# Performance work log

Measured on AMD Instinct MI355X. Metric: run time of the kernel, lower is better.

## Reference

```python
import jax, jax.numpy as jnp
import numpy as np

K = 3          # kernel_size (local window)
PAD = 1        # padding = (K-1)//2 -> 'same' output size
GROUPS = 8
C_OUT = 64


def _unfold3d(x, k):
    """x: [B,C,Dp,Hp,Wp] -> [B,C,D,H,W,kd,kh,kw] sliding windows (stride 1)."""
    B, C, Dp, Hp, Wp = x.shape
    D, H, W = Dp - k + 1, Hp - k + 1, Wp - k + 1
    idx_d = jnp.arange(D)[:, None] + jnp.arange(k)[None, :]
    idx_h = jnp.arange(H)[:, None] + jnp.arange(k)[None, :]
    idx_w = jnp.arange(W)[:, None] + jnp.arange(k)[None, :]
    x = x[:, :, idx_d]              # [B,C,D,kd,Hp,Wp]
    x = x[:, :, :, :, idx_h]        # [B,C,D,kd,H,kh,Wp]
    x = x[:, :, :, :, :, :, idx_w]  # [B,C,D,kd,H,kh,W,kw]
    return jnp.transpose(x, (0, 1, 2, 4, 6, 3, 5, 7))


def setup_inputs() -> dict:
    key = jax.random.key(0)
    ks = jax.random.split(key, 7)
    B, Cin, D, H, W = 1, 64, 16, 64, 64
    c3 = C_OUT // 3                 # 21
    rest = C_OUT - 2 * c3           # 22
    fan_out_scale = np.sqrt(2.0 / C_OUT)  # kaiming_normal fan_out, relu
    x = jax.random.normal(ks[0], (B, Cin, D, H, W), dtype=jnp.float32)
    w_q = jax.random.normal(ks[1], (C_OUT, Cin), dtype=jnp.float32) * fan_out_scale
    w_k = jax.random.normal(ks[2], (C_OUT, Cin), dtype=jnp.float32) * fan_out_scale
    w_v = jax.random.normal(ks[3], (C_OUT, Cin), dtype=jnp.float32) * fan_out_scale
    rel_d = jax.random.normal(ks[4], (c3, 1, 1, 1, K, 1, 1), dtype=jnp.float32)
    rel_h = jax.random.normal(ks[5], (c3, 1, 1, 1, 1, K, 1), dtype=jnp.float32)
    rel_w = jax.random.normal(ks[6], (rest, 1, 1, 1, 1, 1, K), dtype=jnp.float32)
    return {"x": x, "w_q": w_q, "w_k": w_k, "w_v": w_v,
            "rel_d": rel_d, "rel_h": rel_h, "rel_w": rel_w}


def reference(x, w_q, w_k, w_v, rel_d, rel_h, rel_w):
    B, Cin, D, H, W = x.shape
    cg = C_OUT // GROUPS
    c3 = C_OUT // 3
    # 1x1x1 convs (bias=False): plain channel mixing. conv(pad(x)) == pad(conv(x)).
    q = jnp.einsum('oc,bcdhw->bodhw', w_q, x)
    k = jnp.einsum('oc,bcdhw->bodhw', w_k, x)
    v = jnp.einsum('oc,bcdhw->bodhw', w_v, x)
    pad = [(0, 0), (0, 0), (PAD, PAD), (PAD, PAD), (PAD, PAD)]
    k = jnp.pad(k, pad)
    v = jnp.pad(v, pad)
    k_win = _unfold3d(k, K)   # [B,Co,D,H,W,kd,kh,kw]
    v_win = _unfold3d(v, K)
    # split relative position bias across channel thirds
    k_win = jnp.concatenate([
        k_win[:, :c3] + rel_d,
        k_win[:, c3:2 * c3] + rel_h,
        k_win[:, 2 * c3:] + rel_w,
    ], axis=1)
    Kv = K * K * K
    k_win = k_win.reshape(B, GROUPS, cg, D, H, W, Kv)
    v_win = v_win.reshape(B, GROUPS, cg, D, H, W, Kv)
    qg = q.reshape(B, GROUPS, cg, D, H, W, 1)
    attn = jax.nn.softmax(qg * k_win, axis=-1)
    out = jnp.einsum('bncdhwk,bncdhwk->bncdhw', attn, v_win)
    return out.reshape(B, C_OUT, D, H, W)
```

## Files before the change

kernel.cpp:

```cpp
#include <hip/hip_runtime.h>

#define SP    65536
#define DD    16
#define HH    64
#define WW    64
#define CIN   64
#define COUT  64

#define XP    132
#define WP    68

#define LOG2E 1.44269504f


__global__ __launch_bounds__(256) void proj(const float* __restrict__ x,
                                            const float* __restrict__ wq,
                                            const float* __restrict__ wk,
                                            const float* __restrict__ wv,
                                            float* __restrict__ q,
                                            float* __restrict__ k,
                                            float* __restrict__ v) {
    __shared__ float xl[CIN][XP];
    __shared__ float wl[COUT][WP];

    const int t  = threadIdx.x;
    const int p0 = blockIdx.x * 128;
    const int m  = blockIdx.y;

    const float* __restrict__ wsel = (m == 0) ? wq : (m == 1) ? wk : wv;
    float* __restrict__       osel = (m == 0) ? q  : (m == 1) ? k  : v;

#pragma unroll
    for (int i = 0; i < 8; ++i) {
        const int f = t + 256 * i;
        const int c = f >> 5, j = f & 31;
        *(float4*)(&xl[c][j * 4]) = *(const float4*)(x + c * SP + p0 + j * 4);
    }
#pragma unroll
    for (int i = 0; i < 4; ++i) {
        const int f = t + 256 * i;
        const int o = f >> 4, j = f & 15;
        *(float4*)(&wl[o][j * 4]) = *(const float4*)(wsel + o * CIN + j * 4);
    }
    __syncthreads();

    const int og    = t >> 5;
    const int pg    = t & 31;
    const int obase = og * 8;
    const int pbase = pg * 4;

    float acc[8][4] = {};
#pragma unroll 2
    for (int c4 = 0; c4 < CIN / 4; ++c4) {
        float4 w4[8], x4[4];
#pragma unroll
        for (int i = 0; i < 8; ++i)
            w4[i] = *(const float4*)(&wl[obase + i][c4 * 4]);
#pragma unroll
        for (int cc = 0; cc < 4; ++cc)
            x4[cc] = *(const float4*)(&xl[c4 * 4 + cc][pbase]);
#pragma unroll
        for (int i = 0; i < 8; ++i) {
            const float* wf = (const float*)&w4[i];
#pragma unroll
            for (int cc = 0; cc < 4; ++cc) {
                const float* xf = (const float*)&x4[cc];
                const float wv_ = wf[cc];
                acc[i][0] = fmaf(wv_, xf[0], acc[i][0]);
                acc[i][1] = fmaf(wv_, xf[1], acc[i][1]);
                acc[i][2] = fmaf(wv_, xf[2], acc[i][2]);
                acc[i][3] = fmaf(wv_, xf[3], acc[i][3]);
            }
        }
    }

#pragma unroll
    for (int i = 0; i < 8; ++i)
        *(float4*)(osel + (obase + i) * SP + p0 + pbase) =
            make_float4(acc[i][0], acc[i][1], acc[i][2], acc[i][3]);
}

__device__ __forceinline__ float dpp_shr1(float x) {
    return __int_as_float(__builtin_amdgcn_mov_dpp(__float_as_int(x), 0x111, 0xf, 0xf, true));
}
__device__ __forceinline__ float dpp_shl1(float x) {
    return __int_as_float(__builtin_amdgcn_mov_dpp(__float_as_int(x), 0x101, 0xf, 0xf, true));
}

template<int AXIS>
__device__ __forceinline__ void attn_tile(const float* __restrict__ kt,
                                          const float* __restrict__ vt,
                                          const float (&ql)[2][4],
                                          float r0, float r1, float r2,
                                          int wg, int h, int dg,
                                          float (&s)[2][4], float (&a)[2][4]) {
#pragma unroll
    for (int nl = 0; nl < 4; ++nl) {
#pragma unroll
        for (int kh = 0; kh < 3; ++kh) {
            const int off = ((dg * 2 + nl) * 10 + h + kh) * 64 + wg * 4;
            const float4 km = *(const float4*)(kt + off);
            const float4 vm = *(const float4*)(vt + off);
            const float kl = dpp_shr1(km.w), kr = dpp_shl1(km.x);
            const float vl = dpp_shr1(vm.w), vr = dpp_shl1(vm.x);
            const float krow[6] = { kl, km.x, km.y, km.z, km.w, kr };
            const float vrow[6] = { vl, vm.x, vm.y, vm.z, vm.w, vr };

            const float rkh = (kh == 0) ? r0 : (kh == 1) ? r1 : r2;

#pragma unroll
            for (int di = 0; di < 2; ++di) {
                const int kd = nl - di;
                if (kd >= 0 && kd < 3) {
                    const float rdd = (kd == 0) ? r0 : (kd == 1) ? r1 : r2;
                    const float rr  = (AXIS == 0) ? rdd : (AXIS == 1) ? rkh : 0.f;
#pragma unroll
                    for (int wi = 0; wi < 4; ++wi) {
                        const float qv = ql[di][wi];
#pragma unroll
                        for (int kw = 0; kw < 3; ++kw) {
                            const float rc = (AXIS == 2)
                                           ? ((kw == 0) ? r0 : (kw == 1) ? r1 : r2)
                                           : rr;
                            const float e = __builtin_amdgcn_exp2f(qv * (krow[wi + kw] + rc));
                            s[di][wi] += e;
                            a[di][wi] = fmaf(e, vrow[wi + kw], a[di][wi]);
                        }
                    }
                }
            }
        }
    }
}

__global__ __launch_bounds__(256) void attn(const float* __restrict__ kbuf,
                                            const float* __restrict__ vbuf,
                                            const float* __restrict__ qbuf,
                                            const float* __restrict__ rel_d,
                                            const float* __restrict__ rel_h,
                                            const float* __restrict__ rel_w,
                                            float* __restrict__ out) {
    __shared__ float kt[60 * 64];
    __shared__ float vt[60 * 64];

    const int dt = blockIdx.x;
    const int ht = blockIdx.y;
    const int o  = blockIdx.z;

    const int d0 = dt * 4;
    const int h0 = ht * 8;
    const int t  = threadIdx.x;

    const float* __restrict__ kc = kbuf + o * SP;
    const float* __restrict__ vc = vbuf + o * SP;

#pragma unroll
    for (int i = 0; i < 8; ++i) {
        const int idx = t + 256 * i;
        if (idx < 1920) {
            const bool isv = idx >= 960;
            const int rem  = isv ? idx - 960 : idx;
            const int row  = rem >> 4;
            const int j    = rem & 15;
            const int nn   = row / 10;
            const int hp   = row - nn * 10;
            const int dpg  = d0 - 1 + nn;
            const int hpg  = h0 - 1 + hp;
            float4 val = make_float4(0.f, 0.f, 0.f, 0.f);
            if ((unsigned)dpg < (unsigned)DD && (unsigned)hpg < (unsigned)HH) {
                const float* src = (isv ? vc : kc) + (dpg * HH + hpg) * WW + j * 4;
                val = *(const float4*)src;
            }
            *(float4*)((isv ? vt : kt) + row * 64 + j * 4) = val;
        }
    }

    const int wg = t & 15;
    const int h  = (t >> 4) & 7;
    const int dg = t >> 7;

    float ql[2][4];
#pragma unroll
    for (int di = 0; di < 2; ++di) {
        const int dabs = d0 + dg * 2 + di;
        const float4 q4 = *(const float4*)(qbuf + o * SP + (dabs * HH + (h0 + h)) * WW + wg * 4);
        ql[di][0] = q4.x * LOG2E; ql[di][1] = q4.y * LOG2E;
        ql[di][2] = q4.z * LOG2E; ql[di][3] = q4.w * LOG2E;
    }

    __syncthreads();

    float s[2][4] = {};
    float a[2][4] = {};

    if (o < 21) {
        attn_tile<0>(kt, vt, ql, rel_d[o * 3 + 0], rel_d[o * 3 + 1], rel_d[o * 3 + 2],
                     wg, h, dg, s, a);
    } else if (o < 42) {
        const int b = o - 21;
        attn_tile<1>(kt, vt, ql, rel_h[b * 3 + 0], rel_h[b * 3 + 1], rel_h[b * 3 + 2],
                     wg, h, dg, s, a);
    } else {
        const int b = o - 42;
        attn_tile<2>(kt, vt, ql, rel_w[b * 3 + 0], rel_w[b * 3 + 1], rel_w[b * 3 + 2],
                     wg, h, dg, s, a);
    }

#pragma unroll
    for (int di = 0; di < 2; ++di) {
        const int dabs = d0 + dg * 2 + di;
        float4 ov;
        ov.x = a[di][0] * __builtin_amdgcn_rcpf(s[di][0]);
        ov.y = a[di][1] * __builtin_amdgcn_rcpf(s[di][1]);
        ov.z = a[di][2] * __builtin_amdgcn_rcpf(s[di][2]);
        ov.w = a[di][3] * __builtin_amdgcn_rcpf(s[di][3]);
        *(float4*)(out + o * SP + (dabs * HH + (h0 + h)) * WW + wg * 4) = ov;
    }
}

extern "C" void kernel_launch(void* const* d_in, const int* in_sizes, int n_in,
                              void* d_out, int out_size, void* d_ws, size_t ws_size,
                              hipStream_t stream) {
    const float* x     = (const float*)d_in[0];
    const float* w_q   = (const float*)d_in[1];
    const float* w_k   = (const float*)d_in[2];
    const float* w_v   = (const float*)d_in[3];
    const float* rel_d = (const float*)d_in[4];
    const float* rel_h = (const float*)d_in[5];
    const float* rel_w = (const float*)d_in[6];
    float* out = (float*)d_out;

    float* ws = (float*)d_ws;
    float* q  = ws;
    float* k  = ws + (size_t)COUT * SP;
    float* v  = ws + 2 * (size_t)COUT * SP;

    proj<<<dim3(SP / 128, 3), 256, 0, stream>>>(x, w_q, w_k, w_v, q, k, v);
    attn<<<dim3(4, 8, 64), 256, 0, stream>>>(k, v, q, rel_d, rel_h, rel_w, out);
}
```

Measured before the change: 123.8 us.

## Use split-bf16 MFMA for 1x1x1 projection GEMM and fold log2e into q

Rewrites the projection kernel to split x and the weights into high and low bf16 parts and compute the channel-mixing GEMM with three bf16 MFMA products per tile (hi*hi, hi*lo, lo*hi), which approximates fp32 accuracy on the matrix units instead of scalar FMAs. The tile shrinks to 64 spatial positions per block, so the grid doubles. The log2e scaling of q moves from the attention kernel into the projection epilogue. This adds conversion overhead in the staging phase and slightly lower precision than true fp32. The output stores become scalar, with each lane writing one float per row.

```diff
diff --git a/kernel.cpp b/kernel.cpp
--- a/kernel.cpp
+++ b/kernel.cpp
@@ -7,11 +7,19 @@
 #define CIN   64
 #define COUT  64
 
-#define XP    132
-#define WP    68
-
 #define LOG2E 1.44269504f
 
+
+typedef __attribute__((ext_vector_type(8))) short bf16x8;
+typedef __attribute__((ext_vector_type(4))) float f32x4;
+
+__device__ __forceinline__ unsigned short f2bf(float f) {
+    const unsigned u = __float_as_uint(f);
+    return (unsigned short)((u + 0x7FFFu + ((u >> 16) & 1u)) >> 16);
+}
+__device__ __forceinline__ float bf2f(unsigned short h) {
+    return __uint_as_float((unsigned)h << 16);
+}
 
 __global__ __launch_bounds__(256) void proj(const float* __restrict__ x,
                                             const float* __restrict__ wq,
@@ -20,64 +28,90 @@
                                             float* __restrict__ q,
                                             float* __restrict__ k,
                                             float* __restrict__ v) {
-    __shared__ float xl[CIN][XP];
-    __shared__ float wl[COUT][WP];
+    __shared__ __align__(16) unsigned short xh [64][72];
+    __shared__ __align__(16) unsigned short xlo[64][72];
+    __shared__ __align__(16) unsigned short wh [64][72];
+    __shared__ __align__(16) unsigned short wlo[64][72];
 
     const int t  = threadIdx.x;
-    const int p0 = blockIdx.x * 128;
+    const int p0 = blockIdx.x * 64;
     const int m  = blockIdx.y;
 
     const float* __restrict__ wsel = (m == 0) ? wq : (m == 1) ? wk : wv;
     float* __restrict__       osel = (m == 0) ? q  : (m == 1) ? k  : v;
 
 #pragma unroll
-    for (int i = 0; i < 8; ++i) {
-        const int f = t + 256 * i;
-        const int c = f >> 5, j = f & 31;
-        *(float4*)(&xl[c][j * 4]) = *(const float4*)(x + c * SP + p0 + j * 4);
+    for (int i = 0; i < 2; ++i) {
+        const int f  = t + 256 * i;
+        const int c2 = (f >> 4) * 2;
+        const int jj = f & 15;
+        const float4 a = *(const float4*)(x + c2 * SP + p0 + jj * 4);
+        const float4 b = *(const float4*)(x + (c2 + 1) * SP + p0 + jj * 4);
+        const float* af = (const float*)&a;
+        const float* bf = (const float*)&b;
+#pragma unroll
+        for (int e = 0; e < 4; ++e) {
+            const int j = jj * 4 + e;
+            const unsigned short ah = f2bf(af[e]);
+            const unsigned short bh = f2bf(bf[e]);
+            const unsigned short al = f2bf(af[e] - bf2f(ah));
+            const unsigned short bl = f2bf(bf[e] - bf2f(bh));
+            *(unsigned*)&xh [j][c2] = (unsigned)ah | ((unsigned)bh << 16);
+            *(unsigned*)&xlo[j][c2] = (unsigned)al | ((unsigned)bl << 16);
+        }
     }
 #pragma unroll
     for (int i = 0; i < 4; ++i) {
-        const int f = t + 256 * i;
-        const int o = f >> 4, j = f & 15;
-        *(float4*)(&wl[o][j * 4]) = *(const float4*)(wsel + o * CIN + j * 4);
+        const int f  = t + 256 * i;
+        const int o  = f >> 4;
+        const int jj = f & 15;
+        const float4 w4 = *(const float4*)(wsel + o * CIN + jj * 4);
+        const float* wf = (const float*)&w4;
+        unsigned short h0 = f2bf(wf[0]), h1 = f2bf(wf[1]);
+        unsigned short h2 = f2bf(wf[2]), h3 = f2bf(wf[3]);
+        unsigned short l0 = f2bf(wf[0] - bf2f(h0)), l1 = f2bf(wf[1] - bf2f(h1));
+        unsigned short l2 = f2bf(wf[2] - bf2f(h2)), l3 = f2bf(wf[3] - bf2f(h3));
+        *(uint2*)&wh [o][jj * 4] = make_uint2((unsigned)h0 | ((unsigned)h1 << 16),
+                                              (unsigned)h2 | ((unsigned)h3 << 16));
+        *(uint2*)&wlo[o][jj * 4] = make_uint2((unsigned)l0 | ((unsigned)l1 << 16),
+                                              (unsigned)l2 | ((unsigned)l3 << 16));
     }
     __syncthreads();
 
-    const int og    = t >> 5;
-    const int pg    = t & 31;
-    const int obase = og * 8;
-    const int pbase = pg * 4;
-
-    float acc[8][4] = {};
-#pragma unroll 2
-    for (int c4 = 0; c4 < CIN / 4; ++c4) {
-        float4 w4[8], x4[4];
-#pragma unroll
-        for (int i = 0; i < 8; ++i)
-            w4[i] = *(const float4*)(&wl[obase + i][c4 * 4]);
-#pragma unroll
-        for (int cc = 0; cc < 4; ++cc)
-            x4[cc] = *(const float4*)(&xl[c4 * 4 + cc][pbase]);
-#pragma unroll
-        for (int i = 0; i < 8; ++i) {
-            const float* wf = (const float*)&w4[i];
-#pragma unroll
-            for (int cc = 0; cc < 4; ++cc) {
-                const float* xf = (const float*)&x4[cc];
-                const float wv_ = wf[cc];
-                acc[i][0] = fmaf(wv_, xf[0], acc[i][0]);
-                acc[i][1] = fmaf(wv_, xf[1], acc[i][1]);
-                acc[i][2] = fmaf(wv_, xf[2], acc[i][2]);
-                acc[i][3] = fmaf(wv_, xf[3], acc[i][3]);
-            }
-        }
-    }
-
-#pragma unroll
-    for (int i = 0; i < 8; ++i)
-        *(float4*)(osel + (obase + i) * SP + p0 + pbase) =
-            make_float4(acc[i][0], acc[i][1], acc[i][2], acc[i][3]);
+    const int lane  = t & 63;
+    const int wid   = t >> 6;
+    const int lo16  = lane & 15;
+    const int lg    = lane >> 4;
+    const int otile = wid * 16;
+
+    const bf16x8 Ah0 = *(const bf16x8*)&wh [otile + lo16][lg * 8];
+    const bf16x8 Ah1 = *(const bf16x8*)&wh [otile + lo16][32 + lg * 8];
+    const bf16x8 Al0 = *(const bf16x8*)&wlo[otile + lo16][lg * 8];
+    const bf16x8 Al1 = *(const bf16x8*)&wlo[otile + lo16][32 + lg * 8];
+
+    const float scale = (m == 0) ? LOG2E : 1.f;
+
+#pragma unroll
+    for (int jt = 0; jt < 4; ++jt) {
+        const int jr = jt * 16 + lo16;
+        const bf16x8 Bh0 = *(const bf16x8*)&xh [jr][lg * 8];
+        const bf16x8 Bl0 = *(const bf16x8*)&xlo[jr][lg * 8];
+        const bf16x8 Bh1 = *(const bf16x8*)&xh [jr][32 + lg * 8];
+        const bf16x8 Bl1 = *(const bf16x8*)&xlo[jr][32 + lg * 8];
+        f32x4 hh = {0.f, 0.f, 0.f, 0.f};
+        f32x4 hl = {0.f, 0.f, 0.f, 0.f};
+        f32x4 lh = {0.f, 0.f, 0.f, 0.f};
+        hh = __builtin_amdgcn_mfma_f32_16x16x32_bf16(Ah0, Bh0, hh, 0, 0, 0);
+        hl = __builtin_amdgcn_mfma_f32_16x16x32_bf16(Ah0, Bl0, hl, 0, 0, 0);
+        lh = __builtin_amdgcn_mfma_f32_16x16x32_bf16(Al0, Bh0, lh, 0, 0, 0);
+        hh = __builtin_amdgcn_mfma_f32_16x16x32_bf16(Ah1, Bh1, hh, 0, 0, 0);
+        hl = __builtin_amdgcn_mfma_f32_16x16x32_bf16(Ah1, Bl1, hl, 0, 0, 0);
+        lh = __builtin_amdgcn_mfma_f32_16x16x32_bf16(Al1, Bh1, lh, 0, 0, 0);
+        float* op = osel + (otile + lg * 4) * SP + p0 + jt * 16 + lo16;
+#pragma unroll
+        for (int r = 0; r < 4; ++r)
+            op[r * SP] = (hh[r] + hl[r] + lh[r]) * scale;
+    }
 }
 
 __device__ __forceinline__ float dpp_shr1(float x) {
@@ -184,8 +218,8 @@
     for (int di = 0; di < 2; ++di) {
         const int dabs = d0 + dg * 2 + di;
         const float4 q4 = *(const float4*)(qbuf + o * SP + (dabs * HH + (h0 + h)) * WW + wg * 4);
-        ql[di][0] = q4.x * LOG2E; ql[di][1] = q4.y * LOG2E;
-        ql[di][2] = q4.z * LOG2E; ql[di][3] = q4.w * LOG2E;
+        ql[di][0] = q4.x; ql[di][1] = q4.y;
+        ql[di][2] = q4.z; ql[di][3] = q4.w;
     }
 
     __syncthreads();
@@ -235,6 +269,6 @@
     float* k  = ws + (size_t)COUT * SP;
     float* v  = ws + 2 * (size_t)COUT * SP;
 
-    proj<<<dim3(SP / 128, 3), 256, 0, stream>>>(x, w_q, w_k, w_v, q, k, v);
+    proj<<<dim3(SP / 64, 3), 256, 0, stream>>>(x, w_q, w_k, w_v, q, k, v);
     attn<<<dim3(4, 8, 64), 256, 0, stream>>>(k, v, q, rel_d, rel_h, rel_w, out);
 }
```

Result: faster. 119.5 us (-3.4%).
